# Kernel tuning notes

Measured on AMD Instinct MI355X. Metric: run time of the kernel, lower is better.

Reference implementation:

```python
import jax, jax.numpy as jnp
import numpy as np

B, N, M = 2, 2048, 128
H, D = 16, 64
IN_DIM, CTX_DIM = 1024, 768


def layernorm(x, g, b, eps=1e-5):
    mu = x.mean(-1, keepdims=True)
    var = ((x - mu) ** 2).mean(-1, keepdims=True)
    return (x - mu) * jax.lax.rsqrt(var + eps) * g + b


def setup_inputs() -> dict:
    key = jax.random.key(0)
    ks = jax.random.split(key, 8)
    w = lambda i, sh: jax.random.normal(ks[i], sh, jnp.float32) * 0.02
    return {
        "x": jax.random.normal(ks[0], (B, N, IN_DIM), jnp.float32),
        "c_emb": jax.random.normal(ks[1], (B, M, CTX_DIM), jnp.float32),
        "ln_g": jnp.ones((IN_DIM,), jnp.float32),
        "ln_b": jnp.zeros((IN_DIM,), jnp.float32),
        "ctx_ln_g": jnp.ones((CTX_DIM,), jnp.float32),
        "ctx_ln_b": jnp.zeros((CTX_DIM,), jnp.float32),
        "W_ctx": w(2, (CTX_DIM, 2 * D)),
        "b_ctx": jnp.zeros((2 * D,), jnp.float32),
        "W_q": w(3, (IN_DIM, H * D)),
        "W_kv": w(4, (IN_DIM, 2 * H * D)),
        "null_kv": jax.random.normal(ks[5], (2, D), jnp.float32),
        "W_out": w(6, (H * D, IN_DIM)),
        "out_ln_g": jnp.ones((IN_DIM,), jnp.float32),
        "out_ln_b": jnp.zeros((IN_DIM,), jnp.float32),
    }


def reference(x, c_emb, ln_g, ln_b, ctx_ln_g, ctx_ln_b, W_ctx, b_ctx,
              W_q, W_kv, null_kv, W_out, out_ln_g, out_ln_b):
    b, n, _ = x.shape
    xn = layernorm(x, ln_g, ln_b)
    q = (xn @ W_q).reshape(b, n, H, D)                      # [b,n,h,d]
    kv = (xn @ W_kv).reshape(b, n, 2, H, D)
    k, v = kv[:, :, 0], kv[:, :, 1]                         # [b,n,h,d]
    # context projected to a single shared-across-heads k and v
    ckv = layernorm(c_emb, ctx_ln_g, ctx_ln_b) @ W_ctx + b_ctx
    ck, cv = jnp.split(ckv, 2, axis=-1)                     # [b,m,d]
    nk = jnp.broadcast_to(null_kv[0], (b, 1, D))
    nv = jnp.broadcast_to(null_kv[1], (b, 1, D))
    k_ext = jnp.concatenate([nk, ck], axis=1)               # [b,m+1,d]
    v_ext = jnp.concatenate([nv, cv], axis=1)
    scale = D ** -0.5
    s_self = jnp.einsum('bnhd,bkhd->bhnk', q, k) * scale    # [b,h,n,n]
    s_ctx = jnp.einsum('bnhd,bkd->bhnk', q, k_ext) * scale  # [b,h,n,m+1]
    w = jax.nn.softmax(jnp.concatenate([s_self, s_ctx], axis=-1), axis=-1)
    w_self, w_ctx = w[..., :n], w[..., n:]
    out = (jnp.einsum('bhnk,bkhd->bnhd', w_self, v)
           + jnp.einsum('bhnk,bkd->bnhd', w_ctx, v_ext))    # [b,n,h,d]
    out = out.reshape(b, n, H * D) @ W_out                  # [b,n,input_dim]
    return layernorm(out, out_ln_g, out_ln_b)
```

## Files before the change

### kernel.cpp

```cpp
#include <hip/hip_runtime.h>
#include <cstdint>
#include <cstddef>

typedef __attribute__((ext_vector_type(8))) short bf16x8;
typedef __attribute__((ext_vector_type(4))) short bf16x4;
typedef __attribute__((ext_vector_type(4))) float f32x4;
typedef __attribute__((ext_vector_type(4))) unsigned int u32x4;
typedef __attribute__((ext_vector_type(2))) unsigned int u32x2;

__device__ inline unsigned short f2b(float f){
  unsigned int u = __float_as_uint(f);
  u += 0x7fffu + ((u >> 16) & 1u);
  return (unsigned short)(u >> 16);
}
__device__ inline unsigned int pk2(float a, float b){
  unsigned int ua = __float_as_uint(a) + 0x8000u;
  unsigned int ub = __float_as_uint(b) + 0x8000u;
  return __builtin_amdgcn_perm(ub, ua, 0x07060302u);
}
__device__ inline void gl2lds16(const void* g, void* l){
  __builtin_amdgcn_global_load_lds(
      (const __attribute__((address_space(1))) unsigned int*)g,
      (__attribute__((address_space(3))) unsigned int*)l, 16, 0, 0);
}

#define QSCALE 0.18033688011112042f

__global__ __launch_bounds__(256) void wcvt_kernel(
    const float* __restrict__ Wq, const float* __restrict__ Wkv,
    const float* __restrict__ Wout,
    unsigned short* __restrict__ Wqkv_t, unsigned short* __restrict__ Wout_t)
{
  __shared__ short tile[64*72];
  int cg0 = blockIdx.x * 64;
  int kt  = blockIdx.y * 64;
  const float* src; int ld; int col0; unsigned short* dst; int drow0;
  if (cg0 < 1024)      { src = Wq;   ld = 1024; col0 = cg0;        dst = Wqkv_t; drow0 = cg0; }
  else if (cg0 < 3072) { src = Wkv;  ld = 2048; col0 = cg0 - 1024; dst = Wqkv_t; drow0 = cg0; }
  else                 { src = Wout; ld = 1024; col0 = cg0 - 3072; dst = Wout_t; drow0 = cg0 - 3072; }
  int t = threadIdx.x;
  #pragma unroll
  for (int i = 0; i < 16; ++i){
    int lin = t + 256*i;
    int k = lin >> 6, c = lin & 63;
    tile[k*72 + c] = (short)f2b(src[(size_t)(kt + k)*ld + col0 + c]);
  }
  __syncthreads();
  #pragma unroll
  for (int i = 0; i < 16; ++i){
    int lin = t + 256*i;
    int c = lin >> 6, k = lin & 63;
    dst[(size_t)(drow0 + c)*1024 + kt + k] = (unsigned short)tile[k*72 + c];
  }
}

template<bool BF16OUT>
__global__ __launch_bounds__(256) void ln1024_kernel(
    const float* __restrict__ X, const float* __restrict__ G,
    const float* __restrict__ Bb, void* __restrict__ out)
{
  int row = blockIdx.x, t = threadIdx.x;
  float4 x = ((const float4*)(X + (size_t)row*1024))[t];
  float s  = x.x + x.y + x.z + x.w;
  float s2 = x.x*x.x + x.y*x.y + x.z*x.z + x.w*x.w;
  #pragma unroll
  for (int o = 32; o > 0; o >>= 1){ s += __shfl_down(s, o); s2 += __shfl_down(s2, o); }
  __shared__ float red[8];
  int w = t >> 6;
  if ((t & 63) == 0){ red[w] = s; red[4 + w] = s2; }
  __syncthreads();
  float mu  = (red[0]+red[1]+red[2]+red[3]) * (1.0f/1024.0f);
  float var = (red[4]+red[5]+red[6]+red[7]) * (1.0f/1024.0f) - mu*mu;
  float rstd = rsqrtf(var + 1e-5f);
  float4 g = ((const float4*)G)[t];
  float4 b = ((const float4*)Bb)[t];
  float y0 = (x.x-mu)*rstd*g.x + b.x;
  float y1 = (x.y-mu)*rstd*g.y + b.y;
  float y2 = (x.z-mu)*rstd*g.z + b.z;
  float y3 = (x.w-mu)*rstd*g.w + b.w;
  if (BF16OUT){
    ushort4 u; u.x = f2b(y0); u.y = f2b(y1); u.z = f2b(y2); u.w = f2b(y3);
    ((ushort4*)out)[(size_t)row*256 + t] = u;
  } else {
    float4 y; y.x = y0; y.y = y1; y.z = y2; y.w = y3;
    ((float4*)out)[(size_t)row*256 + t] = y;
  }
}

__global__ __launch_bounds__(128) void ctx_kernel(
    const float* __restrict__ Cemb, const float* __restrict__ G,
    const float* __restrict__ Bb, const float* __restrict__ Wctx,
    const float* __restrict__ bctx,
    unsigned short* __restrict__ kext, unsigned short* __restrict__ vext_t)
{
  int row = blockIdx.x;
  int b = row >> 7, m = row & 127;
  const float* xr = Cemb + (size_t)row*768;
  int t = threadIdx.x;
  float v[6]; float s = 0.f, s2 = 0.f;
  #pragma unroll
  for (int j = 0; j < 6; ++j){ float xv = xr[t + 128*j]; v[j] = xv; s += xv; s2 += xv*xv; }
  #pragma unroll
  for (int o = 32; o > 0; o >>= 1){ s += __shfl_down(s, o); s2 += __shfl_down(s2, o); }
  __shared__ float red[4];
  __shared__ float xn[768];
  int w = t >> 6;
  if ((t & 63) == 0){ red[w] = s; red[2 + w] = s2; }
  __syncthreads();
  float mu  = (red[0]+red[1]) * (1.0f/768.0f);
  float var = (red[2]+red[3]) * (1.0f/768.0f) - mu*mu;
  float rstd = rsqrtf(var + 1e-5f);
  #pragma unroll
  for (int j = 0; j < 6; ++j){ int c = t + 128*j; xn[c] = (v[j]-mu)*rstd*G[c] + Bb[c]; }
  __syncthreads();
  float acc = bctx[t];
  #pragma unroll 8
  for (int j = 0; j < 768; ++j) acc += xn[j] * Wctx[j*128 + t];
  unsigned short hv = f2b(acc);
  if (t < 64) kext[((size_t)b*192 + 1 + m)*64 + t] = hv;
  else        vext_t[((size_t)b*64 + (t - 64))*192 + 1 + m] = hv;
}

__global__ __launch_bounds__(256) void kvfill_kernel(
    const float* __restrict__ nullkv,
    unsigned short* __restrict__ kext, unsigned short* __restrict__ vext_t)
{
  int id = blockIdx.x*256 + threadIdx.x;
  int b = id / 12288, rem = id % 12288;
  int row = rem >> 6, d = rem & 63;
  if (row == 0){
    kext[((size_t)b*192 + row)*64 + d]   = f2b(nullkv[d]);
    vext_t[((size_t)b*64 + d)*192 + row] = f2b(nullkv[64 + d]);
  } else if (row >= 129){
    kext[((size_t)b*192 + row)*64 + d]   = 0;
    vext_t[((size_t)b*64 + d)*192 + row] = 0;
  }
}

#define GEMM_MAINLOOP(A_, Bt_)                                                  \
  __shared__ __align__(16) short sA[128*32];                                    \
  __shared__ __align__(16) short sB[128*32];                                    \
  int tM = blockIdx.y * 128, tN = blockIdx.x * 128;                             \
  int t = threadIdx.x, w = t >> 6, lane = t & 63;                               \
  int wm = w & 1, wn = w >> 1, lm = lane & 15, q = lane >> 4;                   \
  int srow = w*32 + (lane >> 2);                                                \
  int sk8  = (lane & 3) << 3;                                                   \
  f32x4 acc[4][4] = {};                                                         \
  for (int kk = 0; kk < 1024; kk += 32){                                        \
    __syncthreads();                                                            \
    gl2lds16(A_  + (size_t)(tM + srow     )*1024 + kk + sk8, &sA[(w*32   )*32]);\
    gl2lds16(A_  + (size_t)(tM + srow + 16)*1024 + kk + sk8, &sA[(w*32+16)*32]);\
    gl2lds16(Bt_ + (size_t)(tN + srow     )*1024 + kk + sk8, &sB[(w*32   )*32]);\
    gl2lds16(Bt_ + (size_t)(tN + srow + 16)*1024 + kk + sk8, &sB[(w*32+16)*32]);\
    __syncthreads();                                                            \
    bf16x8 af[4], bfr[4];                                                       \
    _Pragma("unroll")                                                           \
    for (int i = 0; i < 4; ++i){                                                \
      af[i]  = *(const bf16x8*)(&sA[(wm*64 + i*16 + lm)*32 + q*8]);             \
      bfr[i] = *(const bf16x8*)(&sB[(wn*64 + i*16 + lm)*32 + q*8]);             \
    }                                                                           \
    _Pragma("unroll")                                                           \
    for (int i = 0; i < 4; ++i){                                                \
      _Pragma("unroll")                                                         \
      for (int j = 0; j < 4; ++j)                                               \
        acc[i][j] = __builtin_amdgcn_mfma_f32_16x16x32_bf16(af[i], bfr[j], acc[i][j], 0, 0, 0); \
    }                                                                           \
  }

__global__ __launch_bounds__(256) void gemm_qkv_kernel(
    const unsigned short* __restrict__ A, const unsigned short* __restrict__ Bt,
    unsigned short* __restrict__ Qb, unsigned short* __restrict__ Kb,
    unsigned short* __restrict__ VtG)
{
  GEMM_MAINLOOP(A, Bt)
  if (tN < 1024){
    #pragma unroll
    for (int i = 0; i < 4; ++i){
      int R0 = tM + wm*64 + i*16 + q*4;
      int b = R0 >> 11, n = R0 & 2047;
      #pragma unroll
      for (int j = 0; j < 4; ++j){
        int Cg = tN + wn*64 + j*16 + lm;
        int h = Cg >> 6, d = Cg & 63;
        size_t base = ((((size_t)(b*16 + h) << 11) | n) << 6) + d;
        #pragma unroll
        for (int r = 0; r < 4; ++r)
          Qb[base + (size_t)r*64] = f2b(acc[i][j][r] * QSCALE);
      }
    }
  } else if (tN < 2048){
    #pragma unroll
    for (int i = 0; i < 4; ++i){
      int R0 = tM + wm*64 + i*16 + q*4;
      int b = R0 >> 11, n = R0 & 2047;
      #pragma unroll
      for (int j = 0; j < 4; ++j){
        int c2 = tN - 1024 + wn*64 + j*16 + lm;
        int h = c2 >> 6, d = c2 & 63;
        size_t base = ((((size_t)(b*16 + h) << 11) | n) << 6) + d;
        #pragma unroll
        for (int r = 0; r < 4; ++r)
          Kb[base + (size_t)r*64] = f2b(acc[i][j][r]);
      }
    }
  } else {
    #pragma unroll
    for (int i = 0; i < 4; ++i){
      int R0 = tM + wm*64 + i*16 + q*4;
      int b = R0 >> 11, n = R0 & 2047;
      #pragma unroll
      for (int j = 0; j < 4; ++j){
        int c2 = tN - 2048 + wn*64 + j*16 + lm;
        int h = c2 >> 6, d = c2 & 63;
        ushort4 u;
        u.x = f2b(acc[i][j][0]); u.y = f2b(acc[i][j][1]);
        u.z = f2b(acc[i][j][2]); u.w = f2b(acc[i][j][3]);
        *(ushort4*)(VtG + ((size_t)(b*16 + h)*64 + d)*2048 + n) = u;
      }
    }
  }
}

__global__ __launch_bounds__(256) void gemm_out_kernel(
    const unsigned short* __restrict__ A, const unsigned short* __restrict__ Bt,
    float* __restrict__ C)
{
  GEMM_MAINLOOP(A, Bt)
  #pragma unroll
  for (int i = 0; i < 4; ++i){
    int R0 = tM + wm*64 + i*16 + q*4;
    #pragma unroll
    for (int j = 0; j < 4; ++j){
      int Cg = tN + wn*64 + j*16 + lm;
      #pragma unroll
      for (int r = 0; r < 4; ++r)
        C[(size_t)(R0 + r)*1024 + Cg] = acc[i][j][r];
    }
  }
}

__global__ __launch_bounds__(256) void attn_kernel(
    const unsigned short* __restrict__ Qb, const unsigned short* __restrict__ Kb,
    const unsigned short* __restrict__ VtG, const unsigned short* __restrict__ kext,
    const unsigned short* __restrict__ vext_t, unsigned short* __restrict__ Ob)
{
  __shared__ __align__(16) short sK[64*72];
  __shared__ __align__(16) short sVt[64*72];
  __shared__ __align__(16) short sP[4*32*68];
  int id = blockIdx.x;
  int xcd = id & 7, slot = id >> 3;
  int bh = xcd*4 + (slot >> 4);
  int qt = slot & 15;
  int b = bh >> 4, h = bh & 15;
  int t = threadIdx.x, w = t >> 6, lane = t & 63;
  int lm = lane & 15, q = lane >> 4;

  const unsigned short* Qbase = Qb + ((size_t)bh*2048 + qt*128 + w*32)*64;
  bf16x8 qf[2][2];
  #pragma unroll
  for (int qq = 0; qq < 2; ++qq){
    qf[qq][0] = *(const bf16x8*)(Qbase + (size_t)(qq*16 + lm)*64 + q*8);
    qf[qq][1] = *(const bf16x8*)(Qbase + (size_t)(qq*16 + lm)*64 + q*8 + 32);
  }

  f32x4 o[4][2] = {};
  float l_i[2] = {0.f, 0.f};
  short* pw = &sP[w*2176];

  int r0 = t >> 2, c0 = (t & 3) << 4;
  u32x4 kr0, kr1, vr0, vr1;
  {
    const unsigned short* kp = Kb + ((size_t)bh*2048 + r0)*64 + c0;
    kr0 = *(const u32x4*)kp; kr1 = *(const u32x4*)(kp + 8);
    const unsigned short* vp = VtG + ((size_t)bh*64 + r0)*2048 + c0;
    vr0 = *(const u32x4*)vp; vr1 = *(const u32x4*)(vp + 8);
  }

  for (int tile = 0; tile < 35; ++tile){
    __syncthreads();
    *(u32x4*)(&sK[r0*72 + c0])      = kr0;
    *(u32x4*)(&sK[r0*72 + c0 + 8])  = kr1;
    *(u32x4*)(&sVt[r0*72 + c0])     = vr0;
    *(u32x4*)(&sVt[r0*72 + c0 + 8]) = vr1;
    __syncthreads();

    if (tile + 1 < 35){
      int nt = tile + 1;
      bool ext = nt >= 32;
      int kb = ext ? (nt - 32)*64 : nt*64;
      const unsigned short* kp = ext ? (kext + ((size_t)b*192 + kb + r0)*64 + c0)
                                     : (Kb + ((size_t)bh*2048 + kb + r0)*64 + c0);
      kr0 = *(const u32x4*)kp; kr1 = *(const u32x4*)(kp + 8);
      const unsigned short* vp = ext ? (vext_t + ((size_t)b*64 + r0)*192 + kb + c0)
                                     : (VtG + ((size_t)bh*64 + r0)*2048 + kb + c0);
      vr0 = *(const u32x4*)vp; vr1 = *(const u32x4*)(vp + 8);
    }

    f32x4 s[2][4];
    #pragma unroll
    for (int st = 0; st < 4; ++st){
      bf16x8 kf0 = *(const bf16x8*)(&sK[(st*16 + lm)*72 + q*8]);
      bf16x8 kf1 = *(const bf16x8*)(&sK[(st*16 + lm)*72 + q*8 + 32]);
      #pragma unroll
      for (int qq = 0; qq < 2; ++qq){
        f32x4 z = {};
        z = __builtin_amdgcn_mfma_f32_16x16x32_bf16(kf0, qf[qq][0], z, 0, 0, 0);
        s[qq][st] = __builtin_amdgcn_mfma_f32_16x16x32_bf16(kf1, qf[qq][1], z, 0, 0, 0);
      }
    }
    if (tile == 34){
      #pragma unroll
      for (int st = 0; st < 4; ++st)
        #pragma unroll
        for (int r = 0; r < 4; ++r){
          int key = 128 + st*16 + q*4 + r;
          if (key >= 129){ s[0][st][r] = -1e30f; s[1][st][r] = -1e30f; }
        }
    }

    #pragma unroll
    for (int qq = 0; qq < 2; ++qq){
      float sm = 0.f;
      #pragma unroll
      for (int st = 0; st < 4; ++st)
        #pragma unroll
        for (int r = 0; r < 4; ++r){
          float p = __builtin_amdgcn_exp2f(s[qq][st][r]);
          s[qq][st][r] = p; sm += p;
        }
      l_i[qq] += sm;
      #pragma unroll
      for (int st = 0; st < 4; ++st){
        u32x2 pkd;
        pkd[0] = pk2(s[qq][st][0], s[qq][st][1]);
        pkd[1] = pk2(s[qq][st][2], s[qq][st][3]);
        *(u32x2*)(&pw[(qq*16 + lm)*68 + st*16 + q*4]) = pkd;
      }
    }

    bf16x8 pb[2][2];
    #pragma unroll
    for (int qq = 0; qq < 2; ++qq){
      bf16x4 a0 = *(const bf16x4*)(&pw[(qq*16 + lm)*68 + q*8]);
      bf16x4 a1 = *(const bf16x4*)(&pw[(qq*16 + lm)*68 + q*8 + 4]);
      bf16x4 a2 = *(const bf16x4*)(&pw[(qq*16 + lm)*68 + 32 + q*8]);
      bf16x4 a3 = *(const bf16x4*)(&pw[(qq*16 + lm)*68 + 32 + q*8 + 4]);
      pb[qq][0] = __builtin_shufflevector(a0, a1, 0,1,2,3,4,5,6,7);
      pb[qq][1] = __builtin_shufflevector(a2, a3, 0,1,2,3,4,5,6,7);
    }
    #pragma unroll
    for (int ds = 0; ds < 4; ++ds){
      bf16x8 af0 = *(const bf16x8*)(&sVt[(ds*16 + lm)*72 + q*8]);
      bf16x8 af1 = *(const bf16x8*)(&sVt[(ds*16 + lm)*72 + q*8 + 32]);
      #pragma unroll
      for (int qq = 0; qq < 2; ++qq){
        o[ds][qq] = __builtin_amdgcn_mfma_f32_16x16x32_bf16(af0, pb[qq][0], o[ds][qq], 0, 0, 0);
        o[ds][qq] = __builtin_amdgcn_mfma_f32_16x16x32_bf16(af1, pb[qq][1], o[ds][qq], 0, 0, 0);
      }
    }
  }

  #pragma unroll
  for (int qq = 0; qq < 2; ++qq){
    float l = l_i[qq];
    l += __shfl_xor(l, 16);
    l += __shfl_xor(l, 32);
    float inv = 1.0f / l;
    int n = qt*128 + w*32 + qq*16 + lm;
    size_t base = ((size_t)b*2048 + n)*1024 + h*64 + q*4;
    #pragma unroll
    for (int ds = 0; ds < 4; ++ds){
      ushort4 u;
      u.x = f2b(o[ds][qq][0] * inv); u.y = f2b(o[ds][qq][1] * inv);
      u.z = f2b(o[ds][qq][2] * inv); u.w = f2b(o[ds][qq][3] * inv);
      *(ushort4*)(Ob + base + ds*16) = u;
    }
  }
}

extern "C" void kernel_launch(void* const* d_in, const int* in_sizes, int n_in,
                              void* d_out, int out_size, void* d_ws, size_t ws_size,
                              hipStream_t stream)
{
  const float* x       = (const float*)d_in[0];
  const float* c_emb   = (const float*)d_in[1];
  const float* ln_g    = (const float*)d_in[2];
  const float* ln_b    = (const float*)d_in[3];
  const float* ctx_g   = (const float*)d_in[4];
  const float* ctx_b   = (const float*)d_in[5];
  const float* W_ctx   = (const float*)d_in[6];
  const float* b_ctx   = (const float*)d_in[7];
  const float* W_q     = (const float*)d_in[8];
  const float* W_kv    = (const float*)d_in[9];
  const float* null_kv = (const float*)d_in[10];
  const float* W_out   = (const float*)d_in[11];
  const float* oln_g   = (const float*)d_in[12];
  const float* oln_b   = (const float*)d_in[13];
  float* out = (float*)d_out;

  char* p = (char*)d_ws;
  unsigned short* xn     = (unsigned short*)p; p += (size_t)4096*1024*2;
  unsigned short* Wqkv_t = (unsigned short*)p; p += (size_t)3072*1024*2;
  unsigned short* Wout_t = (unsigned short*)p; p += (size_t)1024*1024*2;
  unsigned short* Qb     = (unsigned short*)p; p += (size_t)32*2048*64*2;
  unsigned short* Kb     = (unsigned short*)p; p += (size_t)32*2048*64*2;
  unsigned short* VtG    = (unsigned short*)p; p += (size_t)32*64*2048*2;
  unsigned short* kext   = (unsigned short*)p; p += (size_t)2*192*64*2;
  unsigned short* vext_t = (unsigned short*)p; p += (size_t)2*64*192*2;
  unsigned short* aout   = (unsigned short*)p; p += (size_t)4096*1024*2;
  float*          ptmp   = (float*)p;          p += (size_t)4096*1024*4;

  wcvt_kernel<<<dim3(64,16), 256, 0, stream>>>(W_q, W_kv, W_out, Wqkv_t, Wout_t);
  ln1024_kernel<true><<<4096, 256, 0, stream>>>(x, ln_g, ln_b, (void*)xn);
  ctx_kernel<<<256, 128, 0, stream>>>(c_emb, ctx_g, ctx_b, W_ctx, b_ctx, kext, vext_t);
  kvfill_kernel<<<96, 256, 0, stream>>>(null_kv, kext, vext_t);
  gemm_qkv_kernel<<<dim3(24,32), 256, 0, stream>>>(xn, Wqkv_t, Qb, Kb, VtG);
  attn_kernel<<<512, 256, 0, stream>>>(Qb, Kb, VtG, kext, vext_t, aout);
  gemm_out_kernel<<<dim3(8,32), 256, 0, stream>>>(aout, Wout_t, ptmp);
  ln1024_kernel<false><<<4096, 256, 0, stream>>>(ptmp, oln_g, oln_b, (void*)out);
}
```

Before: 285.5 us.

## Widen GEMM K-tile with swizzled LDS, remap blocks per XCD, restructure attention waves

The GEMM main loop now stages 64-wide K slices with an XOR-swizzled LDS layout, which halves the number of barriers and is meant to cut bank conflicts. Its 1D grid is remapped so blocks on the same XCD share A rows. The attention kernel moves to 128-thread blocks where each wave owns 64 query rows and reuses K fragments across four query groups, at the cost of higher register pressure. The null/pad fill of kext/vext is folded into ctx_kernel, which removes one launch.

```diff
diff --git a/kernel.cpp b/kernel.cpp
--- a/kernel.cpp
+++ b/kernel.cpp
@@ -90,13 +90,23 @@
 __global__ __launch_bounds__(128) void ctx_kernel(
     const float* __restrict__ Cemb, const float* __restrict__ G,
     const float* __restrict__ Bb, const float* __restrict__ Wctx,
-    const float* __restrict__ bctx,
+    const float* __restrict__ bctx, const float* __restrict__ nullkv,
     unsigned short* __restrict__ kext, unsigned short* __restrict__ vext_t)
 {
   int row = blockIdx.x;
   int b = row >> 7, m = row & 127;
+  int t = threadIdx.x;
+  if (row < 128){
+    int b2 = row >> 6, fr = row & 63;
+    int frow = (fr == 0) ? 0 : (128 + fr);
+    if (t < 64){
+      kext[((size_t)b2*192 + frow)*64 + t] = (frow == 0) ? f2b(nullkv[t]) : (unsigned short)0;
+    } else {
+      int d = t - 64;
+      vext_t[((size_t)b2*64 + d)*192 + frow] = (frow == 0) ? f2b(nullkv[64 + d]) : (unsigned short)0;
+    }
+  }
   const float* xr = Cemb + (size_t)row*768;
-  int t = threadIdx.x;
   float v[6]; float s = 0.f, s2 = 0.f;
   #pragma unroll
   for (int j = 0; j < 6; ++j){ float xv = xr[t + 128*j]; v[j] = xv; s += xv; s2 += xv*xv; }
@@ -121,50 +131,45 @@
   else        vext_t[((size_t)b*64 + (t - 64))*192 + 1 + m] = hv;
 }
 
-__global__ __launch_bounds__(256) void kvfill_kernel(
-    const float* __restrict__ nullkv,
-    unsigned short* __restrict__ kext, unsigned short* __restrict__ vext_t)
-{
-  int id = blockIdx.x*256 + threadIdx.x;
-  int b = id / 12288, rem = id % 12288;
-  int row = rem >> 6, d = rem & 63;
-  if (row == 0){
-    kext[((size_t)b*192 + row)*64 + d]   = f2b(nullkv[d]);
-    vext_t[((size_t)b*64 + d)*192 + row] = f2b(nullkv[64 + d]);
-  } else if (row >= 129){
-    kext[((size_t)b*192 + row)*64 + d]   = 0;
-    vext_t[((size_t)b*64 + d)*192 + row] = 0;
-  }
-}
-
-#define GEMM_MAINLOOP(A_, Bt_)                                                  \
-  __shared__ __align__(16) short sA[128*32];                                    \
-  __shared__ __align__(16) short sB[128*32];                                    \
-  int tM = blockIdx.y * 128, tN = blockIdx.x * 128;                             \
+#define GEMM_MAINLOOP(A_, Bt_, tM_, tN_)                                        \
+  __shared__ __align__(16) short sA[128*64];                                    \
+  __shared__ __align__(16) short sB[128*64];                                    \
   int t = threadIdx.x, w = t >> 6, lane = t & 63;                               \
   int wm = w & 1, wn = w >> 1, lm = lane & 15, q = lane >> 4;                   \
-  int srow = w*32 + (lane >> 2);                                                \
-  int sk8  = (lane & 3) << 3;                                                   \
+  int grow = lane >> 3;                                                         \
+  int gchk = ((lane & 7) ^ grow) << 3;                                          \
   f32x4 acc[4][4] = {};                                                         \
-  for (int kk = 0; kk < 1024; kk += 32){                                        \
+  const unsigned short* Aw = A_ + (size_t)(tM_ + w*32 + grow)*1024 + gchk;      \
+  const unsigned short* Bw = Bt_ + (size_t)(tN_ + w*32 + grow)*1024 + gchk;     \
+  for (int kk = 0; kk < 1024; kk += 64){                                        \
     __syncthreads();                                                            \
-    gl2lds16(A_  + (size_t)(tM + srow     )*1024 + kk + sk8, &sA[(w*32   )*32]);\
-    gl2lds16(A_  + (size_t)(tM + srow + 16)*1024 + kk + sk8, &sA[(w*32+16)*32]);\
-    gl2lds16(Bt_ + (size_t)(tN + srow     )*1024 + kk + sk8, &sB[(w*32   )*32]);\
-    gl2lds16(Bt_ + (size_t)(tN + srow + 16)*1024 + kk + sk8, &sB[(w*32+16)*32]);\
+    gl2lds16(Aw + kk,            &sA[(w*32     )*64]);                          \
+    gl2lds16(Aw + kk +  8*1024,  &sA[(w*32 +  8)*64]);                          \
+    gl2lds16(Aw + kk + 16*1024,  &sA[(w*32 + 16)*64]);                          \
+    gl2lds16(Aw + kk + 24*1024,  &sA[(w*32 + 24)*64]);                          \
+    gl2lds16(Bw + kk,            &sB[(w*32     )*64]);                          \
+    gl2lds16(Bw + kk +  8*1024,  &sB[(w*32 +  8)*64]);                          \
+    gl2lds16(Bw + kk + 16*1024,  &sB[(w*32 + 16)*64]);                          \
+    gl2lds16(Bw + kk + 24*1024,  &sB[(w*32 + 24)*64]);                          \
     __syncthreads();                                                            \
-    bf16x8 af[4], bfr[4];                                                       \
+    bf16x8 af[4][2], bfr[4][2];                                                 \
     _Pragma("unroll")                                                           \
     for (int i = 0; i < 4; ++i){                                                \
-      af[i]  = *(const bf16x8*)(&sA[(wm*64 + i*16 + lm)*32 + q*8]);             \
-      bfr[i] = *(const bf16x8*)(&sB[(wn*64 + i*16 + lm)*32 + q*8]);             \
+      int ra = wm*64 + i*16 + lm, rb = wn*64 + i*16 + lm;                       \
+      _Pragma("unroll")                                                         \
+      for (int hh = 0; hh < 2; ++hh){                                           \
+        int sw = ((hh*4 + q) ^ (lm & 7)) << 3;                                  \
+        af[i][hh]  = *(const bf16x8*)(&sA[ra*64 + sw]);                         \
+        bfr[i][hh] = *(const bf16x8*)(&sB[rb*64 + sw]);                         \
+      }                                                                         \
     }                                                                           \
     _Pragma("unroll")                                                           \
-    for (int i = 0; i < 4; ++i){                                                \
+    for (int hh = 0; hh < 2; ++hh)                                              \
       _Pragma("unroll")                                                         \
-      for (int j = 0; j < 4; ++j)                                               \
-        acc[i][j] = __builtin_amdgcn_mfma_f32_16x16x32_bf16(af[i], bfr[j], acc[i][j], 0, 0, 0); \
-    }                                                                           \
+      for (int i = 0; i < 4; ++i)                                               \
+        _Pragma("unroll")                                                       \
+        for (int j = 0; j < 4; ++j)                                             \
+          acc[i][j] = __builtin_amdgcn_mfma_f32_16x16x32_bf16(af[i][hh], bfr[j][hh], acc[i][j], 0, 0, 0); \
   }
 
 __global__ __launch_bounds__(256) void gemm_qkv_kernel(
@@ -172,7 +177,11 @@
     unsigned short* __restrict__ Qb, unsigned short* __restrict__ Kb,
     unsigned short* __restrict__ VtG)
 {
-  GEMM_MAINLOOP(A, Bt)
+  int id = blockIdx.x;
+  int xcd = id & 7, r = id >> 3;
+  int tM = ((r & 3)*8 + xcd) * 128;
+  int tN = (r >> 2) * 128;
+  GEMM_MAINLOOP(A, Bt, tM, tN)
   if (tN < 1024){
     #pragma unroll
     for (int i = 0; i < 4; ++i){
@@ -184,8 +193,8 @@
         int h = Cg >> 6, d = Cg & 63;
         size_t base = ((((size_t)(b*16 + h) << 11) | n) << 6) + d;
         #pragma unroll
-        for (int r = 0; r < 4; ++r)
-          Qb[base + (size_t)r*64] = f2b(acc[i][j][r] * QSCALE);
+        for (int rr = 0; rr < 4; ++rr)
+          Qb[base + (size_t)rr*64] = f2b(acc[i][j][rr] * QSCALE);
       }
     }
   } else if (tN < 2048){
@@ -199,8 +208,8 @@
         int h = c2 >> 6, d = c2 & 63;
         size_t base = ((((size_t)(b*16 + h) << 11) | n) << 6) + d;
         #pragma unroll
-        for (int r = 0; r < 4; ++r)
-          Kb[base + (size_t)r*64] = f2b(acc[i][j][r]);
+        for (int rr = 0; rr < 4; ++rr)
+          Kb[base + (size_t)rr*64] = f2b(acc[i][j][rr]);
       }
     }
   } else {
@@ -225,7 +234,11 @@
     const unsigned short* __restrict__ A, const unsigned short* __restrict__ Bt,
     float* __restrict__ C)
 {
-  GEMM_MAINLOOP(A, Bt)
+  int id = blockIdx.x;
+  int xcd = id & 7, r = id >> 3;
+  int tM = ((r & 3)*8 + xcd) * 128;
+  int tN = (r >> 2) * 128;
+  GEMM_MAINLOOP(A, Bt, tM, tN)
   #pragma unroll
   for (int i = 0; i < 4; ++i){
     int R0 = tM + wm*64 + i*16 + q*4;
@@ -233,20 +246,20 @@
     for (int j = 0; j < 4; ++j){
       int Cg = tN + wn*64 + j*16 + lm;
       #pragma unroll
-      for (int r = 0; r < 4; ++r)
-        C[(size_t)(R0 + r)*1024 + Cg] = acc[i][j][r];
-    }
-  }
-}
-
-__global__ __launch_bounds__(256) void attn_kernel(
+      for (int rr = 0; rr < 4; ++rr)
+        C[(size_t)(R0 + rr)*1024 + Cg] = acc[i][j][rr];
+    }
+  }
+}
+
+__global__ __launch_bounds__(128, 2) void attn_kernel(
     const unsigned short* __restrict__ Qb, const unsigned short* __restrict__ Kb,
     const unsigned short* __restrict__ VtG, const unsigned short* __restrict__ kext,
     const unsigned short* __restrict__ vext_t, unsigned short* __restrict__ Ob)
 {
   __shared__ __align__(16) short sK[64*72];
   __shared__ __align__(16) short sVt[64*72];
-  __shared__ __align__(16) short sP[4*32*68];
+  __shared__ __align__(16) short sP[2*64*68];
   int id = blockIdx.x;
   int xcd = id & 7, slot = id >> 3;
   int bh = xcd*4 + (slot >> 4);
@@ -255,33 +268,37 @@
   int t = threadIdx.x, w = t >> 6, lane = t & 63;
   int lm = lane & 15, q = lane >> 4;
 
-  const unsigned short* Qbase = Qb + ((size_t)bh*2048 + qt*128 + w*32)*64;
-  bf16x8 qf[2][2];
-  #pragma unroll
-  for (int qq = 0; qq < 2; ++qq){
+  const unsigned short* Qbase = Qb + ((size_t)bh*2048 + qt*128 + w*64)*64;
+  bf16x8 qf[4][2];
+  #pragma unroll
+  for (int qq = 0; qq < 4; ++qq){
     qf[qq][0] = *(const bf16x8*)(Qbase + (size_t)(qq*16 + lm)*64 + q*8);
     qf[qq][1] = *(const bf16x8*)(Qbase + (size_t)(qq*16 + lm)*64 + q*8 + 32);
   }
 
-  f32x4 o[4][2] = {};
-  float l_i[2] = {0.f, 0.f};
-  short* pw = &sP[w*2176];
-
-  int r0 = t >> 2, c0 = (t & 3) << 4;
-  u32x4 kr0, kr1, vr0, vr1;
+  f32x4 o[4][4] = {};
+  float l_i[4] = {0.f, 0.f, 0.f, 0.f};
+  short* pw = &sP[w*64*68];
+
+  int r0 = t >> 1, c0 = (t & 1) << 5;
+  u32x4 kr[4], vr[4];
   {
     const unsigned short* kp = Kb + ((size_t)bh*2048 + r0)*64 + c0;
-    kr0 = *(const u32x4*)kp; kr1 = *(const u32x4*)(kp + 8);
     const unsigned short* vp = VtG + ((size_t)bh*64 + r0)*2048 + c0;
-    vr0 = *(const u32x4*)vp; vr1 = *(const u32x4*)(vp + 8);
+    #pragma unroll
+    for (int jj = 0; jj < 4; ++jj){
+      kr[jj] = *(const u32x4*)(kp + 8*jj);
+      vr[jj] = *(const u32x4*)(vp + 8*jj);
+    }
   }
 
   for (int tile = 0; tile < 35; ++tile){
     __syncthreads();
-    *(u32x4*)(&sK[r0*72 + c0])      = kr0;
-    *(u32x4*)(&sK[r0*72 + c0 + 8])  = kr1;
-    *(u32x4*)(&sVt[r0*72 + c0])     = vr0;
-    *(u32x4*)(&sVt[r0*72 + c0 + 8]) = vr1;
+    #pragma unroll
+    for (int jj = 0; jj < 4; ++jj){
+      *(u32x4*)(&sK[r0*72 + c0 + 8*jj])  = kr[jj];
+      *(u32x4*)(&sVt[r0*72 + c0 + 8*jj]) = vr[jj];
+    }
     __syncthreads();
 
     if (tile + 1 < 35){
@@ -290,57 +307,61 @@
       int kb = ext ? (nt - 32)*64 : nt*64;
       const unsigned short* kp = ext ? (kext + ((size_t)b*192 + kb + r0)*64 + c0)
                                      : (Kb + ((size_t)bh*2048 + kb + r0)*64 + c0);
-      kr0 = *(const u32x4*)kp; kr1 = *(const u32x4*)(kp + 8);
       const unsigned short* vp = ext ? (vext_t + ((size_t)b*64 + r0)*192 + kb + c0)
                                      : (VtG + ((size_t)bh*64 + r0)*2048 + kb + c0);
-      vr0 = *(const u32x4*)vp; vr1 = *(const u32x4*)(vp + 8);
-    }
-
-    f32x4 s[2][4];
+      #pragma unroll
+      for (int jj = 0; jj < 4; ++jj){
+        kr[jj] = *(const u32x4*)(kp + 8*jj);
+        vr[jj] = *(const u32x4*)(vp + 8*jj);
+      }
+    }
+
+    bf16x8 kf[4][2];
     #pragma unroll
     for (int st = 0; st < 4; ++st){
-      bf16x8 kf0 = *(const bf16x8*)(&sK[(st*16 + lm)*72 + q*8]);
-      bf16x8 kf1 = *(const bf16x8*)(&sK[(st*16 + lm)*72 + q*8 + 32]);
-      #pragma unroll
-      for (int qq = 0; qq < 2; ++qq){
+      kf[st][0] = *(const bf16x8*)(&sK[(st*16 + lm)*72 + q*8]);
+      kf[st][1] = *(const bf16x8*)(&sK[(st*16 + lm)*72 + q*8 + 32]);
+    }
+
+    #pragma unroll
+    for (int qq = 0; qq < 4; ++qq){
+      f32x4 s[4];
+      #pragma unroll
+      for (int st = 0; st < 4; ++st){
         f32x4 z = {};
-        z = __builtin_amdgcn_mfma_f32_16x16x32_bf16(kf0, qf[qq][0], z, 0, 0, 0);
-        s[qq][st] = __builtin_amdgcn_mfma_f32_16x16x32_bf16(kf1, qf[qq][1], z, 0, 0, 0);
-      }
-    }
-    if (tile == 34){
+        z = __builtin_amdgcn_mfma_f32_16x16x32_bf16(kf[st][0], qf[qq][0], z, 0, 0, 0);
+        s[st] = __builtin_amdgcn_mfma_f32_16x16x32_bf16(kf[st][1], qf[qq][1], z, 0, 0, 0);
+      }
+      if (tile == 34){
+        #pragma unroll
+        for (int st = 0; st < 4; ++st)
+          #pragma unroll
+          for (int rr = 0; rr < 4; ++rr){
+            int key = 128 + st*16 + q*4 + rr;
+            if (key >= 129) s[st][rr] = -1e30f;
+          }
+      }
+      float sm = 0.f;
       #pragma unroll
       for (int st = 0; st < 4; ++st)
         #pragma unroll
-        for (int r = 0; r < 4; ++r){
-          int key = 128 + st*16 + q*4 + r;
-          if (key >= 129){ s[0][st][r] = -1e30f; s[1][st][r] = -1e30f; }
-        }
-    }
-
-    #pragma unroll
-    for (int qq = 0; qq < 2; ++qq){
-      float sm = 0.f;
-      #pragma unroll
-      for (int st = 0; st < 4; ++st)
-        #pragma unroll
-        for (int r = 0; r < 4; ++r){
-          float p = __builtin_amdgcn_exp2f(s[qq][st][r]);
-          s[qq][st][r] = p; sm += p;
+        for (int rr = 0; rr < 4; ++rr){
+          float p = __builtin_amdgcn_exp2f(s[st][rr]);
+          s[st][rr] = p; sm += p;
         }
       l_i[qq] += sm;
       #pragma unroll
       for (int st = 0; st < 4; ++st){
         u32x2 pkd;
-        pkd[0] = pk2(s[qq][st][0], s[qq][st][1]);
-        pkd[1] = pk2(s[qq][st][2], s[qq][st][3]);
+        pkd[0] = pk2(s[st][0], s[st][1]);
+        pkd[1] = pk2(s[st][2], s[st][3]);
         *(u32x2*)(&pw[(qq*16 + lm)*68 + st*16 + q*4]) = pkd;
       }
     }
 
-    bf16x8 pb[2][2];
-    #pragma unroll
-    for (int qq = 0; qq < 2; ++qq){
+    bf16x8 pb[4][2];
+    #pragma unroll
+    for (int qq = 0; qq < 4; ++qq){
       bf16x4 a0 = *(const bf16x4*)(&pw[(qq*16 + lm)*68 + q*8]);
       bf16x4 a1 = *(const bf16x4*)(&pw[(qq*16 + lm)*68 + q*8 + 4]);
       bf16x4 a2 = *(const bf16x4*)(&pw[(qq*16 + lm)*68 + 32 + q*8]);
@@ -353,7 +374,7 @@
       bf16x8 af0 = *(const bf16x8*)(&sVt[(ds*16 + lm)*72 + q*8]);
       bf16x8 af1 = *(const bf16x8*)(&sVt[(ds*16 + lm)*72 + q*8 + 32]);
       #pragma unroll
-      for (int qq = 0; qq < 2; ++qq){
+      for (int qq = 0; qq < 4; ++qq){
         o[ds][qq] = __builtin_amdgcn_mfma_f32_16x16x32_bf16(af0, pb[qq][0], o[ds][qq], 0, 0, 0);
         o[ds][qq] = __builtin_amdgcn_mfma_f32_16x16x32_bf16(af1, pb[qq][1], o[ds][qq], 0, 0, 0);
       }
@@ -361,12 +382,12 @@
   }
 
   #pragma unroll
-  for (int qq = 0; qq < 2; ++qq){
+  for (int qq = 0; qq < 4; ++qq){
     float l = l_i[qq];
     l += __shfl_xor(l, 16);
     l += __shfl_xor(l, 32);
     float inv = 1.0f / l;
-    int n = qt*128 + w*32 + qq*16 + lm;
+    int n = qt*128 + w*64 + qq*16 + lm;
     size_t base = ((size_t)b*2048 + n)*1024 + h*64 + q*4;
     #pragma unroll
     for (int ds = 0; ds < 4; ++ds){
@@ -412,10 +433,9 @@
 
   wcvt_kernel<<<dim3(64,16), 256, 0, stream>>>(W_q, W_kv, W_out, Wqkv_t, Wout_t);
   ln1024_kernel<true><<<4096, 256, 0, stream>>>(x, ln_g, ln_b, (void*)xn);
-  ctx_kernel<<<256, 128, 0, stream>>>(c_emb, ctx_g, ctx_b, W_ctx, b_ctx, kext, vext_t);
-  kvfill_kernel<<<96, 256, 0, stream>>>(null_kv, kext, vext_t);
-  gemm_qkv_kernel<<<dim3(24,32), 256, 0, stream>>>(xn, Wqkv_t, Qb, Kb, VtG);
-  attn_kernel<<<512, 256, 0, stream>>>(Qb, Kb, VtG, kext, vext_t, aout);
-  gemm_out_kernel<<<dim3(8,32), 256, 0, stream>>>(aout, Wout_t, ptmp);
+  ctx_kernel<<<256, 128, 0, stream>>>(c_emb, ctx_g, ctx_b, W_ctx, b_ctx, null_kv, kext, vext_t);
+  gemm_qkv_kernel<<<768, 256, 0, stream>>>(xn, Wqkv_t, Qb, Kb, VtG);
+  attn_kernel<<<512, 128, 0, stream>>>(Qb, Kb, VtG, kext, vext_t, aout);
+  gemm_out_kernel<<<256, 256, 0, stream>>>(aout, Wout_t, ptmp);
   ln1024_kernel<false><<<4096, 256, 0, stream>>>(ptmp, oln_g, oln_b, (void*)out);
 }
```

Result: no change. 289.1 us (+1.3%).
